# Kernel optimization log

Hardware: AMD Instinct MI355X
Metric: run time of the kernel (lower is better)

Reference implementation:

```python
import jax, jax.numpy as jnp
import numpy as np

FEATURE_DIM = 512
NUM_HEADS = 8
HEAD_DIM = FEATURE_DIM // NUM_HEADS
B, L = 4, 2048


def setup_inputs() -> dict:
    key = jax.random.key(0)
    ks = jax.random.split(key, 10)
    s = 1.0 / np.sqrt(FEATURE_DIM)
    inp = {
        "ppg": jax.random.normal(ks[0], (B, FEATURE_DIM, L), dtype=jnp.float32),
        "ecg": jax.random.normal(ks[1], (B, FEATURE_DIM, L), dtype=jnp.float32),
        "Wq": jax.random.uniform(ks[2], (FEATURE_DIM, FEATURE_DIM), jnp.float32, -s, s),
        "bq": jnp.zeros((FEATURE_DIM,), jnp.float32),
        "Wk": jax.random.uniform(ks[3], (FEATURE_DIM, FEATURE_DIM), jnp.float32, -s, s),
        "bk": jnp.zeros((FEATURE_DIM,), jnp.float32),
        "Wv": jax.random.uniform(ks[4], (FEATURE_DIM, FEATURE_DIM), jnp.float32, -s, s),
        "bv": jnp.zeros((FEATURE_DIM,), jnp.float32),
        "Wo": jax.random.uniform(ks[5], (FEATURE_DIM, FEATURE_DIM), jnp.float32, -s, s),
        "bo": jnp.zeros((FEATURE_DIM,), jnp.float32),
    }
    return inp


def reference(ppg, ecg, Wq, bq, Wk, bk, Wv, bv, Wo, bo):
    # ppg/ecg: (B, C, L) -> (B, L, C)
    x = jnp.transpose(ppg, (0, 2, 1))
    y = jnp.transpose(ecg, (0, 2, 1))
    q = x @ Wq.T + bq  # (B, L, C)
    k = y @ Wk.T + bk
    v = y @ Wv.T + bv
    # split heads: (B, H, L, D)
    def split(t):
        return jnp.transpose(t.reshape(B, L, NUM_HEADS, HEAD_DIM), (0, 2, 1, 3))
    qh, kh, vh = split(q), split(k), split(v)
    scores = jnp.einsum('bhqd,bhkd->bhqk', qh, kh) / jnp.sqrt(jnp.float32(HEAD_DIM))
    probs = jax.nn.softmax(scores, axis=-1)  # dropout is identity in eval mode
    ctx = jnp.einsum('bhqk,bhkd->bhqd', probs, vh)
    ctx = jnp.transpose(ctx, (0, 2, 1, 3)).reshape(B, L, FEATURE_DIM)
    out = ctx @ Wo.T + bo + x  # residual with transposed ppg
    return jnp.transpose(out, (0, 2, 1))  # (B, C, L)
```

## Files before the change

### kernel.cpp

```cpp
#include <hip/hip_runtime.h>
#include <hip/hip_bf16.h>

static constexpr int Bc = 4;
static constexpr int Lc = 2048;
static constexpr int Cc = 512;
static constexpr int Hc = 8;
static constexpr int Dc = 64;

using short8  = __attribute__((ext_vector_type(8))) short;
using float4v = __attribute__((ext_vector_type(4))) float;
using f32x16  = __attribute__((ext_vector_type(16))) float;

static __device__ __forceinline__ unsigned short f2bf(float f) {
    __hip_bfloat16 h = __float2bfloat16(f);
    return *reinterpret_cast<unsigned short*>(&h);
}
static __device__ __forceinline__ float bf2f(unsigned short u) {
    return __uint_as_float(((unsigned int)u) << 16);
}

static __device__ __forceinline__ void gll16(const unsigned short* g, unsigned short* l) {
    __builtin_amdgcn_global_load_lds(
        (const __attribute__((address_space(1))) unsigned int*)g,
        (__attribute__((address_space(3))) unsigned int*)l,
        16, 0, 0);
}

__global__ __launch_bounds__(256) void prep_kernel(
    const float* __restrict__ ppg, const float* __restrict__ ecg,
    const float* __restrict__ Wq, const float* __restrict__ Wk,
    const float* __restrict__ Wv, const float* __restrict__ Wo,
    unsigned short* __restrict__ Xt_ppg, unsigned short* __restrict__ Xt_ecg,
    unsigned short* __restrict__ Wbf)
{
    __shared__ float Ts[64 * 69];
    const int task = blockIdx.x;
    const int tid  = threadIdx.x;

    if (task < 2048) {
        const int src = task >> 10;
        const int rem = task & 1023;
        const int b   = rem >> 8;
        const int c0  = ((rem >> 5) & 7) * 64;
        const int l0  = (rem & 31) * 64;
        const float* X = src ? ecg : ppg;
        unsigned short* Xt = src ? Xt_ecg : Xt_ppg;

        #pragma unroll
        for (int j = 0; j < 4; ++j) {
            int idx = tid + j * 256;
            int c = idx >> 4, l4 = idx & 15;
            float4 v = *(const float4*)(X + ((size_t)b * Cc + c0 + c) * Lc + l0 + l4 * 4);
            Ts[c * 69 + l4 * 4 + 0] = v.x;
            Ts[c * 69 + l4 * 4 + 1] = v.y;
            Ts[c * 69 + l4 * 4 + 2] = v.z;
            Ts[c * 69 + l4 * 4 + 3] = v.w;
        }
        __syncthreads();
        #pragma unroll
        for (int j = 0; j < 8; ++j) {
            int u = tid + j * 256;
            int l = u >> 5, p2 = u & 31;
            float a = Ts[(2 * p2) * 69 + l];
            float bb = Ts[(2 * p2 + 1) * 69 + l];
            ushort2 pk; pk.x = f2bf(a); pk.y = f2bf(bb);
            *(ushort2*)(Xt + ((size_t)b * Lc + l0 + l) * Cc + c0 + 2 * p2) = pk;
        }
    } else {
        const int wb   = task - 2048;
        const int widx = wb >> 7;
        const float* W = widx == 0 ? Wq : widx == 1 ? Wk : widx == 2 ? Wv : Wo;
        size_t off = (size_t)(wb & 127) * 2048 + (size_t)tid * 8;
        float4 v0 = *(const float4*)(W + off);
        float4 v1 = *(const float4*)(W + off + 4);
        unsigned short pk[8] = {f2bf(v0.x), f2bf(v0.y), f2bf(v0.z), f2bf(v0.w),
                                f2bf(v1.x), f2bf(v1.y), f2bf(v1.z), f2bf(v1.w)};
        *(short8*)(Wbf + (size_t)widx * Cc * Cc + off) = *(const short8*)pk;
    }
}

__global__ __launch_bounds__(256) void proj_kernel(
    const unsigned short* __restrict__ Xt_ppg,
    const unsigned short* __restrict__ Xt_ecg,
    const unsigned short* __restrict__ Wbf,
    const float* __restrict__ bq, const float* __restrict__ bk,
    const float* __restrict__ bv,
    unsigned short* __restrict__ Qw, unsigned short* __restrict__ Kw,
    unsigned short* __restrict__ Vtw)
{
    const int z = blockIdx.z, p = z >> 2, b = z & 3;
    const int l0 = blockIdx.x * 128, n0 = blockIdx.y * 128;
    const unsigned short* X = (p == 0) ? Xt_ppg : Xt_ecg;
    const unsigned short* W = Wbf + (size_t)p * Cc * Cc;
    const float* bias = (p == 0) ? bq : (p == 1) ? bk : bv;

    const int tid = threadIdx.x, wave = tid >> 6, lane = tid & 63;
    const int l16 = lane & 15, quad = lane >> 4;
    const int wr = wave >> 1, wc = wave & 1;

    __shared__ __align__(16) unsigned short SH[18432];
    unsigned short* At = SH;
    unsigned short* Bt = SH + 8192;

    float4v acc[4][4] = {};

    const int lrow8 = lane >> 3;
    const int lslot = lane & 7;
    const int sw8   = (lslot ^ lrow8) * 8;

    for (int c0 = 0; c0 < Cc; c0 += 64) {
        #pragma unroll
        for (int i = 0; i < 4; ++i) {
            const int r = wave * 32 + i * 8;
            gll16(X + ((size_t)b * Lc + l0 + r + lrow8) * Cc + c0 + sw8,
                  &At[r * 64]);
            gll16(W + (size_t)(n0 + r + lrow8) * Cc + c0 + sw8,
                  &Bt[r * 64]);
        }
        __syncthreads();

        const unsigned short* Am = (p < 2) ? At : Bt;
        const unsigned short* Bm = (p < 2) ? Bt : At;

        #pragma unroll
        for (int ks = 0; ks < 2; ++ks) {
            const int so = (((ks * 4 + quad) ^ (l16 & 7)) * 8);
            short8 bf[4];
            #pragma unroll
            for (int nt = 0; nt < 4; ++nt)
                bf[nt] = *(const short8*)&Bm[(wc * 64 + nt * 16 + l16) * 64 + so];
            #pragma unroll
            for (int mt = 0; mt < 4; ++mt) {
                short8 af = *(const short8*)&Am[(wr * 64 + mt * 16 + l16) * 64 + so];
                #pragma unroll
                for (int nt = 0; nt < 4; ++nt)
                    acc[mt][nt] = __builtin_amdgcn_mfma_f32_16x16x32_bf16(
                        af, bf[nt], acc[mt][nt], 0, 0, 0);
            }
        }
        __syncthreads();
    }

    constexpr int LDO = 136;
    if (p < 2) {
        const float sc = (p == 0) ? 0.18033688011112042f : 1.0f;
        unsigned short* dst = (p == 0) ? Qw : Kw;
        #pragma unroll
        for (int nt = 0; nt < 4; ++nt) {
            int nl = wc * 64 + nt * 16 + l16;
            float bia = bias[n0 + nl];
            #pragma unroll
            for (int mt = 0; mt < 4; ++mt) {
                #pragma unroll
                for (int r = 0; r < 4; ++r) {
                    int ll = wr * 64 + mt * 16 + quad * 4 + r;
                    SH[ll * LDO + nl] = f2bf((acc[mt][nt][r] + bia) * sc);
                }
            }
        }
        __syncthreads();
        #pragma unroll
        for (int j = 0; j < 8; ++j) {
            int u = tid + j * 256;
            int row = u >> 4, c16 = (u & 15) * 8;
            int l = l0 + row;
            int n = n0 + c16, h = n >> 6, d = n & 63, bh = b * Hc + h;
            *(short8*)(dst + ((size_t)bh * Lc + l) * Dc + d) =
                *(const short8*)&SH[row * LDO + c16];
        }
    } else {
        #pragma unroll
        for (int mt = 0; mt < 4; ++mt) {
            #pragma unroll
            for (int r = 0; r < 4; ++r) {
                int nl = wr * 64 + mt * 16 + quad * 4 + r;
                float bia = bias[n0 + nl];
                #pragma unroll
                for (int nt = 0; nt < 4; ++nt) {
                    int ll = wc * 64 + nt * 16 + l16;
                    SH[nl * LDO + ll] = f2bf(acc[mt][nt][r] + bia);
                }
            }
        }
        __syncthreads();
        #pragma unroll
        for (int j = 0; j < 8; ++j) {
            int u = tid + j * 256;
            int row = u >> 4, c16 = (u & 15) * 8;
            int n = n0 + row, h = n >> 6, d = n & 63, bh = b * Hc + h;
            *(short8*)(Vtw + ((size_t)bh * Dc + d) * Lc + l0 + c16) =
                *(const short8*)&SH[row * LDO + c16];
        }
    }
}

__global__ __launch_bounds__(256, 4) void attn_mfma_kernel(
    const unsigned short* __restrict__ Qg,
    const unsigned short* __restrict__ Kg,
    const unsigned short* __restrict__ Vtg,
    unsigned short* __restrict__ O0,
    unsigned short* __restrict__ O1,
    float* __restrict__ lpart)
{
    const int bid = blockIdx.x;
    const int r8  = bid & 7;
    const int j   = bid >> 3;
    const int g   = (j >> 4) * 8 + r8;
    const int x   = j & 15;
    const int bh    = g >> 1;
    const int split = g & 1;
    const int q0    = x * 128;

    const int tid  = threadIdx.x;
    const int wave = tid >> 6;
    const int lane = tid & 63;
    const int l32  = lane & 31;
    const int hi   = lane >> 5;

    __shared__ __align__(16) unsigned short Kt[2][64 * 64];
    __shared__ __align__(16) unsigned short Vt[2][64 * 64];

    const unsigned short* Kb = Kg  + (size_t)bh * Lc * Dc;
    const unsigned short* Vb = Vtg + (size_t)bh * Dc * Lc;
    const int kbase = split * (Lc / 2);

    short8 qf[4];
    const unsigned short* Qb =
        Qg + ((size_t)bh * Lc + q0 + wave * 32 + l32) * Dc + hi * 8;
    #pragma unroll
    for (int st = 0; st < 4; ++st)
        qf[st] = *(const short8*)(Qb + st * 16);

    const int lrow8 = lane >> 3;
    const int lslot = lane & 7;
    auto STAGE = [&](int buf, int kc) {
        #pragma unroll
        for (int i = 0; i < 2; ++i) {
            const int r = wave * 16 + i * 8 + lrow8;
            const int sw = (lslot ^ (r & 7)) * 8;
            gll16(Kb + (size_t)(kbase + kc + r) * Dc + sw,
                  &Kt[buf][(wave * 16 + i * 8) * 64]);
            gll16(Vb + (size_t)r * Lc + (kbase + kc) + sw,
                  &Vt[buf][(wave * 16 + i * 8) * 64]);
        }
    };

    STAGE(0, 0);
    __syncthreads();

    f32x16 O[2] = {};
    float lsum = 0.0f;

    constexpr int NT = (Lc / 2) / 64;
    for (int it = 0; it < NT; ++it) {
        const int cur = it & 1;
        if (it + 1 < NT) STAGE(cur ^ 1, (it + 1) * 64);

        f32x16 S0, S1;
        #pragma unroll
        for (int e = 0; e < 16; ++e) { S0[e] = 0.0f; S1[e] = 0.0f; }
        #pragma unroll
        for (int st = 0; st < 4; ++st) {
            const int slot = st * 2 + hi;
            short8 k0 = *(const short8*)
                &Kt[cur][l32 * 64 + ((slot ^ (l32 & 7)) * 8)];
            short8 k1 = *(const short8*)
                &Kt[cur][(32 + l32) * 64 + ((slot ^ (l32 & 7)) * 8)];
            S0 = __builtin_amdgcn_mfma_f32_32x32x16_bf16(k0, qf[st], S0, 0, 0, 0);
            S1 = __builtin_amdgcn_mfma_f32_32x32x16_bf16(k1, qf[st], S1, 0, 0, 0);
        }

        #pragma unroll
        for (int kt = 0; kt < 2; ++kt) {
            const f32x16& S = kt ? S1 : S0;
            float p[16];
            #pragma unroll
            for (int e = 0; e < 16; ++e)
                p[e] = __builtin_amdgcn_exp2f(S[e]);
            #pragma unroll
            for (int e = 0; e < 16; e += 4)
                lsum += (p[e] + p[e + 1]) + (p[e + 2] + p[e + 3]);

            unsigned int c[4][2];
            #pragma unroll
            for (int R = 0; R < 4; ++R) {
                #pragma unroll
                for (int w = 0; w < 2; ++w)
                    asm("v_cvt_pk_bf16_f32 %0, %1, %2"
                        : "=v"(c[R][w])
                        : "v"(p[4 * R + 2 * w]), "v"(p[4 * R + 2 * w + 1]));
            }

            #pragma unroll
            for (int ksl = 0; ksl < 2; ++ksl) {
                unsigned int a0 = c[2 * ksl][0],     a1 = c[2 * ksl][1];
                unsigned int a2 = c[2 * ksl + 1][0], a3 = c[2 * ksl + 1][1];
                asm("v_permlane32_swap_b32 %0, %1" : "+v"(a0), "+v"(a2));
                asm("v_permlane32_swap_b32 %0, %1" : "+v"(a1), "+v"(a3));
                union { unsigned int w[4]; short8 s; } u;
                u.w[0] = a0; u.w[1] = a1; u.w[2] = a2; u.w[3] = a3;

                const int ksg = kt * 2 + ksl;
                #pragma unroll
                for (int dt = 0; dt < 2; ++dt) {
                    const int row = dt * 32 + l32;
                    short8 vf = *(const short8*)
                        &Vt[cur][row * 64 + ((((ksg * 2) + hi) ^ (row & 7)) * 8)];
                    O[dt] = __builtin_amdgcn_mfma_f32_32x32x16_bf16(
                        u.s, vf, O[dt], 0, 0, 0);
                }
            }
        }
        if (it + 1 < NT) __syncthreads();
    }

    lsum += __shfl_xor(lsum, 32, 64);
    const int b = bh >> 3, h = bh & 7;
    unsigned short* Om = split ? O1 : O0;
    float* lp = lpart + (size_t)split * (Bc * Hc) * Lc + (size_t)bh * Lc;
    if (hi == 0)
        lp[q0 + wave * 32 + l32] = lsum;

    #pragma unroll
    for (int dt = 0; dt < 2; ++dt) {
        #pragma unroll
        for (int e = 0; e < 16; ++e) {
            const int q = q0 + wave * 32 + (e & 3) + 8 * (e >> 2) + 4 * hi;
            Om[((size_t)b * Lc + q) * Cc + h * Dc + dt * 32 + l32] =
                f2bf(O[dt][e]);
        }
    }
}

__global__ __launch_bounds__(256) void outproj_kernel(
    const unsigned short* __restrict__ O0, const unsigned short* __restrict__ O1,
    const float* __restrict__ lpart,
    const unsigned short* __restrict__ Wo_bf,
    const float* __restrict__ bo, const float* __restrict__ ppg,
    float* __restrict__ out)
{
    constexpr int LDW = 72;
    const int b = blockIdx.z;
    const int l0 = blockIdx.x * 128, n0 = blockIdx.y * 128;
    const int tid = threadIdx.x, wave = tid >> 6, lane = tid & 63;
    const int l16 = lane & 15, quad = lane >> 4;
    const int wr = wave >> 1, wc = wave & 1;

    __shared__ __align__(16) unsigned short At[128 * LDW];
    __shared__ __align__(16) unsigned short Bt[128 * LDW];

    float4v acc[4][4] = {};
    const int srow = tid >> 3, sc8 = tid & 7;
    const size_t lplane = (size_t)(Bc * Hc) * Lc;

    for (int c0 = 0; c0 < Cc; c0 += 64) {
        const int h = c0 >> 6;
        const float* lp0 = lpart + (size_t)(b * Hc + h) * Lc;
        const float* lp1 = lp0 + lplane;

        #pragma unroll
        for (int j = 0; j < 4; ++j) {
            int row = srow + j * 32;
            *(short8*)&At[row * LDW + sc8 * 8] =
                *(const short8*)(Wo_bf + (size_t)(n0 + row) * Cc + c0 + sc8 * 8);
            int l = l0 + row;
            float inv = 1.0f / (lp0[l] + lp1[l]);
            size_t off = ((size_t)b * Lc + l) * Cc + c0 + sc8 * 8;
            short8 a8 = *(const short8*)(O0 + off);
            short8 b8 = *(const short8*)(O1 + off);
            unsigned short pk[8];
            #pragma unroll
            for (int e = 0; e < 8; ++e) {
                unsigned short ua = ((const unsigned short*)&a8)[e];
                unsigned short ub = ((const unsigned short*)&b8)[e];
                pk[e] = f2bf((bf2f(ua) + bf2f(ub)) * inv);
            }
            *(short8*)&Bt[row * LDW + sc8 * 8] = *(const short8*)pk;
        }
        __syncthreads();

        #pragma unroll
        for (int ks = 0; ks < 2; ++ks) {
            short8 bfr[4];
            #pragma unroll
            for (int nt = 0; nt < 4; ++nt)
                bfr[nt] = *(const short8*)&Bt[(wc * 64 + nt * 16 + l16) * LDW
                                              + ks * 32 + quad * 8];
            #pragma unroll
            for (int mt = 0; mt < 4; ++mt) {
                short8 af = *(const short8*)&At[(wr * 64 + mt * 16 + l16) * LDW
                                                + ks * 32 + quad * 8];
                #pragma unroll
                for (int nt = 0; nt < 4; ++nt)
                    acc[mt][nt] = __builtin_amdgcn_mfma_f32_16x16x32_bf16(
                        af, bfr[nt], acc[mt][nt], 0, 0, 0);
            }
        }
        __syncthreads();
    }

    #pragma unroll
    for (int mt = 0; mt < 4; ++mt) {
        #pragma unroll
        for (int r = 0; r < 4; ++r) {
            int n = n0 + wr * 64 + mt * 16 + quad * 4 + r;
            float bia = bo[n];
            #pragma unroll
            for (int nt = 0; nt < 4; ++nt) {
                int l = l0 + wc * 64 + nt * 16 + l16;
                size_t oidx = ((size_t)b * Cc + n) * Lc + l;
                out[oidx] = acc[mt][nt][r] + bia + ppg[oidx];
            }
        }
    }
}

extern "C" void kernel_launch(void* const* d_in, const int* in_sizes, int n_in,
                              void* d_out, int out_size, void* d_ws, size_t ws_size,
                              hipStream_t stream) {
    const float* ppg = (const float*)d_in[0];
    const float* ecg = (const float*)d_in[1];
    const float* Wq  = (const float*)d_in[2];
    const float* bq  = (const float*)d_in[3];
    const float* Wk  = (const float*)d_in[4];
    const float* bk  = (const float*)d_in[5];
    const float* Wv  = (const float*)d_in[6];
    const float* bv  = (const float*)d_in[7];
    const float* Wo  = (const float*)d_in[8];
    const float* bo  = (const float*)d_in[9];
    float* out = (float*)d_out;

    unsigned short* base   = (unsigned short*)d_ws;
    const size_t M = 1024 * 1024;
    unsigned short* Xt_ppg = base;
    unsigned short* Xt_ecg = base + 4 * M;
    unsigned short* Wbf    = base + 8 * M;
    unsigned short* Qw     = base + 9 * M;
    unsigned short* Kw     = base + 13 * M;
    unsigned short* Vtw    = base + 17 * M;
    float* lpart = (float*)(base + 21 * M);
    unsigned short* Opart0 = base;
    unsigned short* Opart1 = base + 4 * M;

    prep_kernel<<<2560, 256, 0, stream>>>(ppg, ecg, Wq, Wk, Wv, Wo,
                                          Xt_ppg, Xt_ecg, Wbf);

    dim3 g1(Lc / 128, Cc / 128, 3 * Bc);
    proj_kernel<<<g1, 256, 0, stream>>>(Xt_ppg, Xt_ecg, Wbf, bq, bk, bv,
                                        Qw, Kw, Vtw);

    attn_mfma_kernel<<<1024, 256, 0, stream>>>(Qw, Kw, Vtw, Opart0, Opart1, lpart);

    dim3 g3(Lc / 128, Cc / 128, Bc);
    outproj_kernel<<<g3, 256, 0, stream>>>(Opart0, Opart1, lpart,
                                           Wbf + (size_t)3 * Cc * Cc,
                                           bo, ppg, out);
}
```

Baseline: 182.0 us.

## Drop KV split in attention, normalize in-kernel, DMA-load outproj tiles

The attention kernel no longer splits the key range across two blocks. Each block now walks all 2048 keys and normalizes its output by the row sum before writing a single bf16 context tensor. This removes the partial-output and lpart writes and the combine/normalize step in the output projection, which now streams Wo and the context straight into swizzled LDS with global_load_lds. The trade-off is half as many attention blocks (512), each with a loop twice as long, which lowers parallelism and latency hiding on a large GPU.

```diff
diff --git a/kernel.cpp b/kernel.cpp
--- a/kernel.cpp
+++ b/kernel.cpp
@@ -198,18 +198,15 @@
     const unsigned short* __restrict__ Qg,
     const unsigned short* __restrict__ Kg,
     const unsigned short* __restrict__ Vtg,
-    unsigned short* __restrict__ O0,
-    unsigned short* __restrict__ O1,
-    float* __restrict__ lpart)
+    unsigned short* __restrict__ Og)
 {
     const int bid = blockIdx.x;
     const int r8  = bid & 7;
     const int j   = bid >> 3;
     const int g   = (j >> 4) * 8 + r8;
     const int x   = j & 15;
-    const int bh    = g >> 1;
-    const int split = g & 1;
-    const int q0    = x * 128;
+    const int bh  = g;
+    const int q0  = x * 128;
 
     const int tid  = threadIdx.x;
     const int wave = tid >> 6;
@@ -222,7 +219,6 @@
 
     const unsigned short* Kb = Kg  + (size_t)bh * Lc * Dc;
     const unsigned short* Vb = Vtg + (size_t)bh * Dc * Lc;
-    const int kbase = split * (Lc / 2);
 
     short8 qf[4];
     const unsigned short* Qb =
@@ -238,9 +234,9 @@
         for (int i = 0; i < 2; ++i) {
             const int r = wave * 16 + i * 8 + lrow8;
             const int sw = (lslot ^ (r & 7)) * 8;
-            gll16(Kb + (size_t)(kbase + kc + r) * Dc + sw,
+            gll16(Kb + (size_t)(kc + r) * Dc + sw,
                   &Kt[buf][(wave * 16 + i * 8) * 64]);
-            gll16(Vb + (size_t)r * Lc + (kbase + kc) + sw,
+            gll16(Vb + (size_t)r * Lc + kc + sw,
                   &Vt[buf][(wave * 16 + i * 8) * 64]);
         }
     };
@@ -251,7 +247,7 @@
     f32x16 O[2] = {};
     float lsum = 0.0f;
 
-    constexpr int NT = (Lc / 2) / 64;
+    constexpr int NT = Lc / 64;
     for (int it = 0; it < NT; ++it) {
         const int cur = it & 1;
         if (it + 1 < NT) STAGE(cur ^ 1, (it + 1) * 64);
@@ -315,81 +311,66 @@
     }
 
     lsum += __shfl_xor(lsum, 32, 64);
+    const float inv = 1.0f / lsum;
+
+    float invq[16];
+    #pragma unroll
+    for (int e = 0; e < 16; ++e)
+        invq[e] = __shfl(inv, (e & 3) + 8 * (e >> 2) + 4 * hi, 64);
+
     const int b = bh >> 3, h = bh & 7;
-    unsigned short* Om = split ? O1 : O0;
-    float* lp = lpart + (size_t)split * (Bc * Hc) * Lc + (size_t)bh * Lc;
-    if (hi == 0)
-        lp[q0 + wave * 32 + l32] = lsum;
-
     #pragma unroll
     for (int dt = 0; dt < 2; ++dt) {
         #pragma unroll
         for (int e = 0; e < 16; ++e) {
             const int q = q0 + wave * 32 + (e & 3) + 8 * (e >> 2) + 4 * hi;
-            Om[((size_t)b * Lc + q) * Cc + h * Dc + dt * 32 + l32] =
-                f2bf(O[dt][e]);
+            Og[((size_t)b * Lc + q) * Cc + h * Dc + dt * 32 + l32] =
+                f2bf(O[dt][e] * invq[e]);
         }
     }
 }
 
 __global__ __launch_bounds__(256) void outproj_kernel(
-    const unsigned short* __restrict__ O0, const unsigned short* __restrict__ O1,
-    const float* __restrict__ lpart,
+    const unsigned short* __restrict__ Og,
     const unsigned short* __restrict__ Wo_bf,
     const float* __restrict__ bo, const float* __restrict__ ppg,
     float* __restrict__ out)
 {
-    constexpr int LDW = 72;
     const int b = blockIdx.z;
     const int l0 = blockIdx.x * 128, n0 = blockIdx.y * 128;
     const int tid = threadIdx.x, wave = tid >> 6, lane = tid & 63;
     const int l16 = lane & 15, quad = lane >> 4;
     const int wr = wave >> 1, wc = wave & 1;
 
-    __shared__ __align__(16) unsigned short At[128 * LDW];
-    __shared__ __align__(16) unsigned short Bt[128 * LDW];
+    __shared__ __align__(16) unsigned short At[128 * 64];
+    __shared__ __align__(16) unsigned short Bt[128 * 64];
 
     float4v acc[4][4] = {};
-    const int srow = tid >> 3, sc8 = tid & 7;
-    const size_t lplane = (size_t)(Bc * Hc) * Lc;
+    const int lrow8 = lane >> 3;
+    const int lslot = lane & 7;
+    const int sw8   = (lslot ^ lrow8) * 8;
 
     for (int c0 = 0; c0 < Cc; c0 += 64) {
-        const int h = c0 >> 6;
-        const float* lp0 = lpart + (size_t)(b * Hc + h) * Lc;
-        const float* lp1 = lp0 + lplane;
-
-        #pragma unroll
-        for (int j = 0; j < 4; ++j) {
-            int row = srow + j * 32;
-            *(short8*)&At[row * LDW + sc8 * 8] =
-                *(const short8*)(Wo_bf + (size_t)(n0 + row) * Cc + c0 + sc8 * 8);
-            int l = l0 + row;
-            float inv = 1.0f / (lp0[l] + lp1[l]);
-            size_t off = ((size_t)b * Lc + l) * Cc + c0 + sc8 * 8;
-            short8 a8 = *(const short8*)(O0 + off);
-            short8 b8 = *(const short8*)(O1 + off);
-            unsigned short pk[8];
-            #pragma unroll
-            for (int e = 0; e < 8; ++e) {
-                unsigned short ua = ((const unsigned short*)&a8)[e];
-                unsigned short ub = ((const unsigned short*)&b8)[e];
-                pk[e] = f2bf((bf2f(ua) + bf2f(ub)) * inv);
-            }
-            *(short8*)&Bt[row * LDW + sc8 * 8] = *(const short8*)pk;
+        #pragma unroll
+        for (int i = 0; i < 4; ++i) {
+            const int r = wave * 32 + i * 8;
+            gll16(Wo_bf + (size_t)(n0 + r + lrow8) * Cc + c0 + sw8,
+                  &At[r * 64]);
+            gll16(Og + ((size_t)b * Lc + l0 + r + lrow8) * Cc + c0 + sw8,
+                  &Bt[r * 64]);
         }
         __syncthreads();
 
         #pragma unroll
         for (int ks = 0; ks < 2; ++ks) {
+            const int so = (((ks * 4 + quad) ^ (l16 & 7)) * 8);
             short8 bfr[4];
             #pragma unroll
             for (int nt = 0; nt < 4; ++nt)
-                bfr[nt] = *(const short8*)&Bt[(wc * 64 + nt * 16 + l16) * LDW
-                                              + ks * 32 + quad * 8];
+                bfr[nt] = *(const short8*)&Bt[(wc * 64 + nt * 16 + l16) * 64 + so];
             #pragma unroll
             for (int mt = 0; mt < 4; ++mt) {
-                short8 af = *(const short8*)&At[(wr * 64 + mt * 16 + l16) * LDW
-                                                + ks * 32 + quad * 8];
+                short8 af = *(const short8*)&At[(wr * 64 + mt * 16 + l16) * 64 + so];
                 #pragma unroll
                 for (int nt = 0; nt < 4; ++nt)
                     acc[mt][nt] = __builtin_amdgcn_mfma_f32_16x16x32_bf16(
@@ -438,9 +419,7 @@
     unsigned short* Qw     = base + 9 * M;
     unsigned short* Kw     = base + 13 * M;
     unsigned short* Vtw    = base + 17 * M;
-    float* lpart = (float*)(base + 21 * M);
-    unsigned short* Opart0 = base;
-    unsigned short* Opart1 = base + 4 * M;
+    unsigned short* Og     = base;
 
     prep_kernel<<<2560, 256, 0, stream>>>(ppg, ecg, Wq, Wk, Wv, Wo,
                                           Xt_ppg, Xt_ecg, Wbf);
@@ -449,10 +428,10 @@
     proj_kernel<<<g1, 256, 0, stream>>>(Xt_ppg, Xt_ecg, Wbf, bq, bk, bv,
                                         Qw, Kw, Vtw);
 
-    attn_mfma_kernel<<<1024, 256, 0, stream>>>(Qw, Kw, Vtw, Opart0, Opart1, lpart);
+    attn_mfma_kernel<<<512, 256, 0, stream>>>(Qw, Kw, Vtw, Og);
 
     dim3 g3(Lc / 128, Cc / 128, Bc);
-    outproj_kernel<<<g3, 256, 0, stream>>>(Opart0, Opart1, lpart,
+    outproj_kernel<<<g3, 256, 0, stream>>>(Og,
                                            Wbf + (size_t)3 * Cc * Cc,
                                            bo, ppg, out);
 }
```

Result: no change. 182.8 us (+0.4%).
